# Performance work log

Measured on AMD Instinct MI355X. Metric: run time of the kernel, lower is better.

The kernel has to match this reference:

```python
import jax, jax.numpy as jnp
import numpy as np
import math

B, T, D, H, L, V = 2, 1024, 768, 12, 4, 50257
HD = D // H
ROPE_PCT = 0.5
MAX_WL = 10000.0
EPS = 1e-5


def setup_inputs() -> dict:
    key = jax.random.key(0)
    ks = jax.random.split(key, 8)
    s = 0.02
    return {
        "idx": jax.random.randint(ks[0], (B, T), 0, V, dtype=jnp.int32),
        "wte": jax.random.normal(ks[1], (V, D), jnp.float32) * s,
        "ln1_g": jnp.ones((L, D), jnp.float32),
        "ln1_b": jnp.zeros((L, D), jnp.float32),
        "Wqkv": jax.random.normal(ks[2], (L, D, 3 * D), jnp.float32) * s,
        "bqkv": jnp.zeros((L, 3 * D), jnp.float32),
        "Wo": jax.random.normal(ks[3], (L, D, D), jnp.float32) * s,
        "bo": jnp.zeros((L, D), jnp.float32),
        "ln2_g": jnp.ones((L, D), jnp.float32),
        "ln2_b": jnp.zeros((L, D), jnp.float32),
        "Wfc": jax.random.normal(ks[4], (L, D, 4 * D), jnp.float32) * s,
        "bfc": jnp.zeros((L, 4 * D), jnp.float32),
        "Wp": jax.random.normal(ks[5], (L, 4 * D, D), jnp.float32) * s,
        "bp": jnp.zeros((L, D), jnp.float32),
        "lnf_g": jnp.ones((D,), jnp.float32),
        "lnf_b": jnp.zeros((D,), jnp.float32),
        "Wlm": jax.random.normal(ks[6], (D, V), jnp.float32) * s,
    }


def _ln(x, g, b):
    m = x.mean(-1, keepdims=True)
    v = x.var(-1, keepdims=True)
    return (x - m) / jnp.sqrt(v + EPS) * g + b


def _gelu(x):
    return 0.5 * x * (1.0 + jnp.tanh(math.sqrt(2.0 / math.pi) * (x + 0.044715 * x ** 3)))


def _p_rope(x, positions):
    # x: [B, H, T, HD]; partial RoPE: rotate first ROPE_PCT of angle pairs, leave rest.
    rope_angles = int(ROPE_PCT * HD // 2)
    nope_angles = HD // 2 - rope_angles
    fraction = 2.0 * jnp.arange(0, rope_angles) / HD
    timescale = jnp.power(MAX_WL, fraction)
    timescale = jnp.pad(timescale, (0, nope_angles), constant_values=jnp.inf)
    sinusoid = positions[:, None] / timescale[None, :]  # [T, HD//2]; pos/inf = 0 -> no rotation
    sin, cos = jnp.sin(sinusoid), jnp.cos(sinusoid)
    first, second = jnp.split(x, 2, axis=-1)
    out = jnp.concatenate([first * cos - second * sin, second * cos + first * sin], axis=-1)
    return out.astype(x.dtype)


def reference(idx, wte, ln1_g, ln1_b, Wqkv, bqkv, Wo, bo, ln2_g, ln2_b, Wfc, bfc, Wp, bp, lnf_g, lnf_b, Wlm):
    x = wte[idx]  # [B, T, D]
    positions = jnp.arange(T, dtype=x.dtype)
    causal = jnp.tril(jnp.ones((T, T), dtype=bool))
    scale = jnp.sqrt(jnp.float32(HD)).astype(x.dtype)
    for l in range(L):
        h1 = _ln(x, ln1_g[l], ln1_b[l])
        h2 = _ln(x, ln2_g[l], ln2_b[l])  # note: both LNs read the same x (as in source)
        # attention
        qkv = h1 @ Wqkv[l] + bqkv[l]
        q, k, v = jnp.split(qkv, 3, axis=-1)
        sh = lambda t: t.reshape(B, T, H, HD).transpose(0, 2, 1, 3)
        q, k, v = sh(q), sh(k), sh(v)
        q = _p_rope(q, positions)
        k = _p_rope(k, positions)
        att = jnp.einsum('bhqd,bhkd->bhqk', q, k) / scale
        att = jnp.where(causal, att, jnp.finfo(att.dtype).min)
        att = jax.nn.softmax(att, axis=-1)
        y = jnp.einsum('bhqk,bhkd->bhqd', att, v)
        y = y.transpose(0, 2, 1, 3).reshape(B, T, D)
        x = x + (y @ Wo[l] + bo[l])
        # MLP
        h = _gelu(h2 @ Wfc[l] + bfc[l])
        x = x + (h @ Wp[l] + bp[l])
    x = _ln(x, lnf_g, lnf_b)
    logits = x @ Wlm  # [B, T, V]
    return logits
```

## Files before the change

### kernel.cpp

```cpp
#include <hip/hip_runtime.h>

typedef unsigned short u16;
typedef unsigned int u32;
typedef __attribute__((ext_vector_type(8))) short bf16x8;
typedef __attribute__((ext_vector_type(4))) float f32x4;

#define SEQ 1024
#define DM 768
#define NH 12
#define HD2 64
#define NLAYER 4
#define NVOCAB 50257
#define BT 2048

__device__ __forceinline__ u16 f2bf(float f) {
  union { float f; u32 u; } v; v.f = f;
  u32 r = v.u + 0x7FFFu + ((v.u >> 16) & 1u);
  return (u16)(r >> 16);
}
__device__ __forceinline__ float bf2f(u16 u) {
  union { u32 u; float f; } v; v.u = ((u32)u) << 16;
  return v.f;
}

__device__ __forceinline__ void glds16(const u16* g, u16* l) {
  __builtin_amdgcn_global_load_lds(
      (const __attribute__((address_space(1))) u32*)(const void*)g,
      (__attribute__((address_space(3))) u32*)(void*)l, 16, 0, 0);
}

__device__ __forceinline__ void cvt_tile(const float* __restrict__ in,
                                         u16* __restrict__ out, int R, int C,
                                         int cx, int ry, u16 (*t)[68]) {
  int c0 = cx * 64, r0 = ry * 64;
  int tx = threadIdx.x & 15, ty = threadIdx.x >> 4;
  int c = c0 + tx * 4;
#pragma unroll
  for (int i = 0; i < 4; ++i) {
    int r = r0 + ty + i * 16;
    float4 v = make_float4(0.f, 0.f, 0.f, 0.f);
    if (c + 3 < C) {
      v = *(const float4*)&in[(size_t)r * C + c];
    } else {
      if (c + 0 < C) v.x = in[(size_t)r * C + c];
      if (c + 1 < C) v.y = in[(size_t)r * C + c + 1];
      if (c + 2 < C) v.z = in[(size_t)r * C + c + 2];
      if (c + 3 < C) v.w = in[(size_t)r * C + c + 3];
    }
    t[ty + i * 16][tx * 4 + 0] = f2bf(v.x);
    t[ty + i * 16][tx * 4 + 1] = f2bf(v.y);
    t[ty + i * 16][tx * 4 + 2] = f2bf(v.z);
    t[ty + i * 16][tx * 4 + 3] = f2bf(v.w);
  }
  __syncthreads();
  int wl = threadIdx.x & 31, grp = threadIdx.x >> 5;
#pragma unroll
  for (int it = 0; it < 8; ++it) {
    int cc = it * 8 + grp;
    int gcol = c0 + cc;
    if (gcol < C) {
      u32 wv = (u32)t[2 * wl][cc] | ((u32)t[2 * wl + 1][cc] << 16);
      *(u32*)&out[(size_t)gcol * R + r0 + 2 * wl] = wv;
    }
  }
}

__global__ void k_prep(const int* __restrict__ idx, const float* __restrict__ wte,
                       float* __restrict__ xf, float* __restrict__ ctab,
                       float* __restrict__ stab, const float* __restrict__ Wqkv,
                       const float* __restrict__ Wo, const float* __restrict__ Wfc,
                       const float* __restrict__ Wp, const float* __restrict__ Wlm,
                       u16* __restrict__ wqkvT, u16* __restrict__ woT,
                       u16* __restrict__ wfcT, u16* __restrict__ wpT,
                       u16* __restrict__ wlmT) {
  __shared__ u16 t[64][68];
  int bid = blockIdx.x;
  if (bid < BT) {
    int tok = idx[bid];
    const float* s = wte + (size_t)tok * DM;
    float* d = xf + (size_t)bid * DM;
    for (int c = threadIdx.x; c < DM; c += 256) d[c] = s[c];
    return;
  }
  bid -= BT;
  if (bid < 64) {
    int gid = bid * 256 + threadIdx.x;
    int tt = gid >> 4, j = gid & 15;
    float inv = powf(10000.f, -(float)j * (1.f / 32.f));
    float ang = (float)tt * inv;
    ctab[gid] = cosf(ang);
    stab[gid] = sinf(ang);
    return;
  }
  bid -= 64;
  if (bid < NLAYER * 1728) {
    int layer = bid / 1728, r = bid % 1728;
    if (r < 432) {
      cvt_tile(Wqkv + (size_t)layer * DM * 3 * DM,
               wqkvT + (size_t)layer * 3 * DM * DM, DM, 3 * DM, r % 36, r / 36, t);
      return;
    }
    r -= 432;
    if (r < 144) {
      cvt_tile(Wo + (size_t)layer * DM * DM, woT + (size_t)layer * DM * DM,
               DM, DM, r % 12, r / 12, t);
      return;
    }
    r -= 144;
    if (r < 576) {
      cvt_tile(Wfc + (size_t)layer * DM * 4 * DM,
               wfcT + (size_t)layer * 4 * DM * DM, DM, 4 * DM, r % 48, r / 48, t);
      return;
    }
    r -= 576;
    cvt_tile(Wp + (size_t)layer * 4 * DM * DM, wpT + (size_t)layer * 4 * DM * DM,
             4 * DM, DM, r % 12, r / 12, t);
    return;
  }
  bid -= NLAYER * 1728;
  cvt_tile(Wlm, wlmT, DM, NVOCAB, bid % 786, bid / 786, t);
}

__global__ void k_ln(const float* __restrict__ x, const float* __restrict__ g1,
                     const float* __restrict__ b1, const float* __restrict__ g2,
                     const float* __restrict__ b2, u16* __restrict__ o1,
                     u16* __restrict__ o2) {
  int w = threadIdx.x >> 6, l = threadIdx.x & 63;
  int r = blockIdx.x * 4 + w;
  const float* xr = x + (size_t)r * DM;
  float2 v[6];
  float s = 0.f;
#pragma unroll
  for (int i = 0; i < 6; ++i) {
    v[i] = *(const float2*)&xr[2 * l + i * 128];
    s += v[i].x + v[i].y;
  }
#pragma unroll
  for (int o = 1; o < 64; o <<= 1) s += __shfl_xor(s, o);
  float mean = s * (1.f / DM);
  float vs = 0.f;
#pragma unroll
  for (int i = 0; i < 6; ++i) {
    float dx = v[i].x - mean, dy = v[i].y - mean;
    vs += dx * dx + dy * dy;
  }
#pragma unroll
  for (int o = 1; o < 64; o <<= 1) vs += __shfl_xor(vs, o);
  float rstd = rsqrtf(vs * (1.f / DM) + 1e-5f);
  u16* p1 = o1 + (size_t)r * DM;
#pragma unroll
  for (int i = 0; i < 6; ++i) {
    int c = 2 * l + i * 128;
    float2 gg = *(const float2*)&g1[c];
    float2 bb = *(const float2*)&b1[c];
    u32 wv = (u32)f2bf((v[i].x - mean) * rstd * gg.x + bb.x) |
             ((u32)f2bf((v[i].y - mean) * rstd * gg.y + bb.y) << 16);
    *(u32*)&p1[c] = wv;
  }
  if (o2) {
    u16* p2 = o2 + (size_t)r * DM;
#pragma unroll
    for (int i = 0; i < 6; ++i) {
      int c = 2 * l + i * 128;
      float2 gg = *(const float2*)&g2[c];
      float2 bb = *(const float2*)&b2[c];
      u32 wv = (u32)f2bf((v[i].x - mean) * rstd * gg.x + bb.x) |
               ((u32)f2bf((v[i].y - mean) * rstd * gg.y + bb.y) << 16);
      *(u32*)&p2[c] = wv;
    }
  }
}

__global__ void k_attn(const u16* __restrict__ qr, const u16* __restrict__ kr,
                       const u16* __restrict__ vT, u16* __restrict__ yb) {
  int ti = (int)gridDim.x - 1 - (int)blockIdx.x;
  int bh = blockIdx.y;
  __shared__ u16 Ps[64 * 72];
  __shared__ u16 Ks[2][4096];
  __shared__ u16 Vs[2][4096];
  int tid = threadIdx.x;
  int rr = tid >> 2, cc = tid & 3;
  int w = tid >> 6, l = tid & 63;
  int rl = l & 15, g = l >> 4;
  {
    const u16* gq = qr + ((size_t)bh * SEQ + ti * 64 + rr) * HD2;
    *(uint4*)&Ps[rr * 72 + cc * 8]      = *(const uint4*)(gq + cc * 8);
    *(uint4*)&Ps[rr * 72 + cc * 8 + 32] = *(const uint4*)(gq + cc * 8 + 32);
  }
  int srow = w * 8 + (l >> 3);
  int gs = (l & 7) ^ (l >> 3);
  const u16* gkb = kr + (size_t)bh * SEQ * HD2;
  const u16* gvb = vT + (size_t)bh * HD2 * SEQ;
  glds16(gkb + (size_t)srow * 64 + gs * 8,        &Ks[0][w * 512]);
  glds16(gkb + (size_t)(32 + srow) * 64 + gs * 8, &Ks[0][2048 + w * 512]);
  glds16(gvb + (size_t)srow * SEQ + gs * 8,       &Vs[0][w * 512]);
  glds16(gvb + (size_t)(32 + srow) * SEQ + gs * 8,&Vs[0][2048 + w * 512]);
  __syncthreads();
  bf16x8 aq0 = *(const bf16x8*)&Ps[(w * 16 + rl) * 72 + g * 8];
  bf16x8 aq1 = *(const bf16x8*)&Ps[(w * 16 + rl) * 72 + 32 + g * 8];
  float m[4], lsum[4];
  f32x4 oacc[4] = {};
#pragma unroll
  for (int r2 = 0; r2 < 4; ++r2) { m[r2] = -3.0e38f; lsum[r2] = 0.f; }
  int qloc = w * 16 + g * 4;
  int sw = rl & 7;
  int cur = 0;
  for (int kt = 0; kt <= ti; ++kt) {
    if (kt < ti) {
      int nx = cur ^ 1;
      glds16(gkb + (size_t)((kt + 1) * 64 + srow) * 64 + gs * 8,      &Ks[nx][w * 512]);
      glds16(gkb + (size_t)((kt + 1) * 64 + 32 + srow) * 64 + gs * 8, &Ks[nx][2048 + w * 512]);
      glds16(gvb + (size_t)srow * SEQ + (kt + 1) * 64 + gs * 8,       &Vs[nx][w * 512]);
      glds16(gvb + (size_t)(32 + srow) * SEQ + (kt + 1) * 64 + gs * 8,&Vs[nx][2048 + w * 512]);
    }
    f32x4 s[4] = {};
    __builtin_amdgcn_s_setprio(1);
#pragma unroll
    for (int nt = 0; nt < 4; ++nt) {
      int r = (nt * 16 + rl) * 64;
      bf16x8 b0 = *(const bf16x8*)&Ks[cur][r + ((0 + g) ^ sw) * 8];
      bf16x8 b1 = *(const bf16x8*)&Ks[cur][r + ((4 + g) ^ sw) * 8];
      s[nt] = __builtin_amdgcn_mfma_f32_16x16x32_bf16(aq0, b0, s[nt], 0, 0, 0);
      s[nt] = __builtin_amdgcn_mfma_f32_16x16x32_bf16(aq1, b1, s[nt], 0, 0, 0);
    }
    __builtin_amdgcn_s_setprio(0);
    if (kt == ti) {
#pragma unroll
      for (int nt = 0; nt < 4; ++nt) {
        int col = nt * 16 + rl;
#pragma unroll
        for (int r2 = 0; r2 < 4; ++r2)
          if (col > qloc + r2) s[nt][r2] = -3.0e38f;
      }
    }
    float lmax[4];
#pragma unroll
    for (int r2 = 0; r2 < 4; ++r2)
      lmax[r2] = fmaxf(fmaxf(s[0][r2], s[1][r2]), fmaxf(s[2][r2], s[3][r2]));
    bool need = (lmax[0] > m[0] + 8.f) || (lmax[1] > m[1] + 8.f) ||
                (lmax[2] > m[2] + 8.f) || (lmax[3] > m[3] + 8.f);
    if (__any(need)) {
#pragma unroll
      for (int r2 = 0; r2 < 4; ++r2) {
        float pm = lmax[r2];
#pragma unroll
        for (int o = 1; o < 16; o <<= 1) pm = fmaxf(pm, __shfl_xor(pm, o));
        if (pm > m[r2] + 8.f) {
          float corr = __expf(m[r2] - pm);
          m[r2] = pm;
          lsum[r2] *= corr;
          oacc[0][r2] *= corr; oacc[1][r2] *= corr;
          oacc[2][r2] *= corr; oacc[3][r2] *= corr;
        }
      }
    }
#pragma unroll
    for (int r2 = 0; r2 < 4; ++r2) {
      float p0 = __expf(s[0][r2] - m[r2]);
      float p1 = __expf(s[1][r2] - m[r2]);
      float p2 = __expf(s[2][r2] - m[r2]);
      float p3 = __expf(s[3][r2] - m[r2]);
      float ps = p0 + p1 + p2 + p3;
#pragma unroll
      for (int o = 1; o < 16; o <<= 1) ps += __shfl_xor(ps, o);
      lsum[r2] += ps;
      int prow = (qloc + r2) * 72;
      Ps[prow + rl]      = f2bf(p0);
      Ps[prow + 16 + rl] = f2bf(p1);
      Ps[prow + 32 + rl] = f2bf(p2);
      Ps[prow + 48 + rl] = f2bf(p3);
    }
    bf16x8 pa0 = *(const bf16x8*)&Ps[(w * 16 + rl) * 72 + g * 8];
    bf16x8 pa1 = *(const bf16x8*)&Ps[(w * 16 + rl) * 72 + 32 + g * 8];
    __builtin_amdgcn_s_setprio(1);
#pragma unroll
    for (int nt = 0; nt < 4; ++nt) {
      int r = (nt * 16 + rl) * 64;
      bf16x8 b0 = *(const bf16x8*)&Vs[cur][r + ((0 + g) ^ sw) * 8];
      bf16x8 b1 = *(const bf16x8*)&Vs[cur][r + ((4 + g) ^ sw) * 8];
      oacc[nt] = __builtin_amdgcn_mfma_f32_16x16x32_bf16(pa0, b0, oacc[nt], 0, 0, 0);
      oacc[nt] = __builtin_amdgcn_mfma_f32_16x16x32_bf16(pa1, b1, oacc[nt], 0, 0, 0);
    }
    __builtin_amdgcn_s_setprio(0);
    __syncthreads();
    cur ^= 1;
  }
  int b = bh / NH, h = bh % NH;
  float invl[4];
#pragma unroll
  for (int r2 = 0; r2 < 4; ++r2) invl[r2] = 1.f / lsum[r2];
#pragma unroll
  for (int nt = 0; nt < 4; ++nt) {
    int d = nt * 16 + rl;
#pragma unroll
    for (int r2 = 0; r2 < 4; ++r2) {
      int trow = ti * 64 + qloc + r2;
      yb[((size_t)(b * SEQ + trow)) * DM + h * HD2 + d] = f2bf(oacc[nt][r2] * invl[r2]);
    }
  }
}

template <int MODE>
__global__ void k_g128(const u16* __restrict__ A, const u16* __restrict__ Bt,
                       float* __restrict__ outf, int M, int N, int K, int MT) {
  __shared__ u16 SM[16384];
  float* cw = (float*)SM;
  int nwg = gridDim.x;
  int id = blockIdx.x;
  if ((nwg & 7) == 0) id = (id & 7) * (nwg >> 3) + (id >> 3);
  int mt = id % MT, nt = id / MT;
  int m0 = mt * 128, n0 = nt * 128;
  int tid = threadIdx.x;
  int w = tid >> 6, l = tid & 63;
  int srow = w * 16 + (l >> 2);
  int gs = (l & 3) ^ ((l >> 3) & 3);
  const u16* gA0 = A + (size_t)(m0 + srow) * K + gs * 8;
  const u16* gA1 = A + (size_t)(m0 + 64 + srow) * K + gs * 8;
  int rb0 = n0 + srow;      if (rb0 > N - 1) rb0 = N - 1;
  int rb1 = n0 + 64 + srow; if (rb1 > N - 1) rb1 = N - 1;
  const u16* gB0 = Bt + (size_t)rb0 * K + gs * 8;
  const u16* gB1 = Bt + (size_t)rb1 * K + gs * 8;
  int wm = (w >> 1) * 64, wn = (w & 1) * 64;
  int rl = l & 15, g = l >> 4;
  int sla = g ^ ((rl >> 1) & 3);
  f32x4 acc[4][4] = {};
  int nK = K >> 5;
  int cur = 0;
  {
    u16* dA = SM + w * 512;
    glds16(gA0, dA); glds16(gA1, dA + 2048);
    u16* dB = SM + 4096 + w * 512;
    glds16(gB0, dB); glds16(gB1, dB + 2048);
  }
  __syncthreads();
  for (int kt = 0; kt < nK; ++kt) {
    if (kt + 1 < nK) {
      u16* dA = SM + (cur ^ 1) * 8192 + w * 512;
      glds16(gA0 + (kt + 1) * 32, dA); glds16(gA1 + (kt + 1) * 32, dA + 2048);
      u16* dB = dA + 4096;
      glds16(gB0 + (kt + 1) * 32, dB); glds16(gB1 + (kt + 1) * 32, dB + 2048);
    }
    const u16* As = SM + cur * 8192;
    const u16* Bs = As + 4096;
    bf16x8 af[4], bfr[4];
    __builtin_amdgcn_s_setprio(1);
#pragma unroll
    for (int i = 0; i < 4; ++i)
      af[i] = *(const bf16x8*)&As[(wm + i * 16 + rl) * 32 + sla * 8];
#pragma unroll
    for (int j = 0; j < 4; ++j)
      bfr[j] = *(const bf16x8*)&Bs[(wn + j * 16 + rl) * 32 + sla * 8];
#pragma unroll
    for (int i = 0; i < 4; ++i)
#pragma unroll
      for (int j = 0; j < 4; ++j)
        acc[i][j] = __builtin_amdgcn_mfma_f32_16x16x32_bf16(af[i], bfr[j],
                                                            acc[i][j], 0, 0, 0);
    __builtin_amdgcn_s_setprio(0);
    __syncthreads();
    cur ^= 1;
  }
#pragma unroll
  for (int ch = 0; ch < 4; ++ch) {
    if ((w >> 1) == (ch >> 1)) {
      int ib = (ch & 1) * 2;
#pragma unroll
      for (int ii = 0; ii < 2; ++ii) {
#pragma unroll
        for (int j = 0; j < 4; ++j) {
          int col = wn + j * 16 + rl;
#pragma unroll
          for (int r2 = 0; r2 < 4; ++r2) {
            int rowc = ii * 16 + g * 4 + r2;
            cw[rowc * 132 + col] = acc[ib + ii][j][r2];
          }
        }
      }
    }
    __syncthreads();
    for (int t = tid; t < 4096; t += 256) {
      int rowc = t >> 7, col = t & 127;
      int gc = n0 + col;
      if (gc < N)
        __builtin_nontemporal_store(cw[rowc * 132 + col],
                                    &outf[(size_t)(m0 + ch * 32 + rowc) * N + gc]);
    }
    __syncthreads();
  }
}

template <int MODE>
__global__ void k_gw(const u16* __restrict__ A, const u16* __restrict__ Bt,
                     const float* __restrict__ bias, u16* __restrict__ outb,
                     int M, int N, int K, int MT,
                     const float* __restrict__ ctab,
                     const float* __restrict__ stab, u16* __restrict__ qrp,
                     u16* __restrict__ krp, u16* __restrict__ vTp) {
  __shared__ u16 SM2[24576];
  float* cw = (float*)SM2;
  int nwg = gridDim.x;
  int id = blockIdx.x;
  if ((nwg & 7) == 0) id = (id & 7) * (nwg >> 3) + (id >> 3);
  int mt = id % MT, nt = id / MT;
  int m0 = mt * 64, n0 = nt * 128;
  int tid = threadIdx.x;
  int w = tid >> 6, l = tid & 63;
  int row0 = tid >> 3, slot0 = tid & 7;
  int gs0 = slot0 ^ (row0 & 7);
  const u16* gA0 = A + (size_t)(m0 + row0) * K + gs0 * 8;
  const u16* gA1 = gA0 + (size_t)32 * K;
  const u16* gB0 = Bt + (size_t)(n0 + row0) * K + gs0 * 8;
  const u16* gB1 = gB0 + (size_t)32 * K;
  const u16* gB2 = gB0 + (size_t)64 * K;
  const u16* gB3 = gB0 + (size_t)96 * K;
  int wm = (w >> 1) * 32, wn = (w & 1) * 64;
  int rl = l & 15, g = l >> 4;
  int sl0 = g ^ (rl & 7), sl1 = (4 + g) ^ (rl & 7);
  f32x4 acc[2][4] = {};
  int nK = K >> 6;
  int cur = 0;
  {
    u16* dA = SM2;
    glds16(gA0, dA + w * 512); glds16(gA1, dA + 2048 + w * 512);
    u16* dB = SM2 + 8192;
    glds16(gB0, dB + w * 512);        glds16(gB1, dB + 2048 + w * 512);
    glds16(gB2, dB + 4096 + w * 512); glds16(gB3, dB + 6144 + w * 512);
  }
  __syncthreads();
  for (int kt = 0; kt < nK; ++kt) {
    if (kt + 1 < nK) {
      int ka = (kt + 1) * 64;
      u16* dA = SM2 + (cur ^ 1) * 4096;
      glds16(gA0 + ka, dA + w * 512); glds16(gA1 + ka, dA + 2048 + w * 512);
      u16* dB = SM2 + 8192 + (cur ^ 1) * 8192;
      glds16(gB0 + ka, dB + w * 512);        glds16(gB1 + ka, dB + 2048 + w * 512);
      glds16(gB2 + ka, dB + 4096 + w * 512); glds16(gB3 + ka, dB + 6144 + w * 512);
    }
    const u16* Ac = SM2 + cur * 4096;
    const u16* Bc = SM2 + 8192 + cur * 8192;
    bf16x8 a0[2], a1[2], b0[4], b1[4];
    __builtin_amdgcn_s_setprio(1);
#pragma unroll
    for (int i = 0; i < 2; ++i) {
      int r = (wm + i * 16 + rl) * 64;
      a0[i] = *(const bf16x8*)&Ac[r + sl0 * 8];
      a1[i] = *(const bf16x8*)&Ac[r + sl1 * 8];
    }
#pragma unroll
    for (int j = 0; j < 4; ++j) {
      int r = (wn + j * 16 + rl) * 64;
      b0[j] = *(const bf16x8*)&Bc[r + sl0 * 8];
      b1[j] = *(const bf16x8*)&Bc[r + sl1 * 8];
    }
#pragma unroll
    for (int i = 0; i < 2; ++i)
#pragma unroll
      for (int j = 0; j < 4; ++j) {
        acc[i][j] = __builtin_amdgcn_mfma_f32_16x16x32_bf16(a0[i], b0[j],
                                                            acc[i][j], 0, 0, 0);
        acc[i][j] = __builtin_amdgcn_mfma_f32_16x16x32_bf16(a1[i], b1[j],
                                                            acc[i][j], 0, 0, 0);
      }
    __builtin_amdgcn_s_setprio(0);
    __syncthreads();
    cur ^= 1;
  }
#pragma unroll
  for (int i = 0; i < 2; ++i) {
#pragma unroll
    for (int j = 0; j < 4; ++j) {
      int col = wn + j * 16 + rl;
      float bv = bias[n0 + col];
#pragma unroll
      for (int r2 = 0; r2 < 4; ++r2) {
        float v = acc[i][j][r2] + bv;
        if (MODE == 1) {
          float u = 0.7978845608028654f * (v + 0.044715f * v * v * v);
          v = 0.5f * v * (1.f + tanhf(u));
        }
        cw[(wm + i * 16 + g * 4 + r2) * 133 + col] = v;
      }
    }
  }
  __syncthreads();
  if (MODE == 1) {
    for (int t = tid; t < 4096; t += 256) {
      int rowc = t >> 6, cp = t & 63;
      u32 wv = (u32)f2bf(cw[rowc * 133 + 2 * cp]) |
               ((u32)f2bf(cw[rowc * 133 + 2 * cp + 1]) << 16);
      *(u32*)&outb[(size_t)(m0 + rowc) * N + n0 + 2 * cp] = wv;
    }
  } else {
    int reg = n0 / DM;
    int h0 = (n0 % DM) / 64;
    int bb = m0 >> 10;
    int t0 = m0 & (SEQ - 1);
    size_t bhb = (size_t)bb * NH + h0;
    if (reg < 2) {
      u16* dst = (reg == 0) ? qrp : krp;
      float qs = (reg == 0) ? 0.125f : 1.f;
      for (int t = tid; t < 4096; t += 256) {
        int rowc = t >> 6, cp = t & 63;
        int c = 2 * cp;
        int hh = c >> 6, d = c & 63;
        int tt = t0 + rowc;
        float x0 = cw[rowc * 133 + c];
        float x1 = cw[rowc * 133 + c + 1];
        float o0, o1;
        if (d < 32) {
          float y0 = cw[rowc * 133 + c + 32];
          float y1 = cw[rowc * 133 + c + 33];
          float c0 = 1.f, s0 = 0.f, c1 = 1.f, s1 = 0.f;
          if (d < 16) {
            c0 = ctab[tt * 16 + d];     s0 = stab[tt * 16 + d];
            c1 = ctab[tt * 16 + d + 1]; s1 = stab[tt * 16 + d + 1];
          }
          o0 = x0 * c0 - y0 * s0;
          o1 = x1 * c1 - y1 * s1;
        } else {
          int j = d - 32;
          float y0 = cw[rowc * 133 + c - 32];
          float y1 = cw[rowc * 133 + c - 31];
          float c0 = 1.f, s0 = 0.f, c1 = 1.f, s1 = 0.f;
          if (j < 16) {
            c0 = ctab[tt * 16 + j];     s0 = stab[tt * 16 + j];
            c1 = ctab[tt * 16 + j + 1]; s1 = stab[tt * 16 + j + 1];
          }
          o0 = x0 * c0 + y0 * s0;
          o1 = x1 * c1 + y1 * s1;
        }
        u32 wv = (u32)f2bf(o0 * qs) | ((u32)f2bf(o1 * qs) << 16);
        *(u32*)&dst[((bhb + hh) * SEQ + tt) * HD2 + d] = wv;
      }
    } else {
      for (int t = tid; t < 4096; t += 256) {
        int dcol = t >> 5, p = t & 31;
        int hh = dcol >> 6, d = dcol & 63;
        int tt = t0 + 2 * p;
        u32 wv = (u32)f2bf(cw[(2 * p) * 133 + dcol]) |
                 ((u32)f2bf(cw[(2 * p + 1) * 133 + dcol]) << 16);
        *(u32*)&vTp[((bhb + hh) * HD2 + d) * SEQ + tt] = wv;
      }
    }
  }
}

__global__ void k_wofc(const u16* __restrict__ yb, const u16* __restrict__ woT,
                       const float* __restrict__ bo, float* __restrict__ xf,
                       const u16* __restrict__ h2b, const u16* __restrict__ wfcT,
                       const float* __restrict__ bfc, u16* __restrict__ hgel) {
  __shared__ u16 SM2[24576];
  int nwg = gridDim.x;
  int id = blockIdx.x;
  id = (id & 7) * (nwg >> 3) + (id >> 3);
  int tid = threadIdx.x;
  int w = tid >> 6, l = tid & 63;
  int rl = l & 15, g = l >> 4;
  int row0 = tid >> 3, slot0 = tid & 7;
  int gs0 = slot0 ^ (row0 & 7);
  int sl0 = g ^ (rl & 7), sl1 = (4 + g) ^ (rl & 7);
  if (id < 768) {
    float* cw = (float*)SM2;
    int mt = id % 32, nt = id / 32;
    int m0 = mt * 64, n0 = nt * 128;
    const int K = DM, N = 4 * DM;
    const u16* gA0 = h2b + (size_t)(m0 + row0) * K + gs0 * 8;
    const u16* gA1 = gA0 + (size_t)32 * K;
    const u16* gB0 = wfcT + (size_t)(n0 + row0) * K + gs0 * 8;
    const u16* gB1 = gB0 + (size_t)32 * K;
    const u16* gB2 = gB0 + (size_t)64 * K;
    const u16* gB3 = gB0 + (size_t)96 * K;
    int wm = (w >> 1) * 32, wn = (w & 1) * 64;
    f32x4 acc[2][4] = {};
    int nK = K >> 6;
    int cur = 0;
    {
      u16* dA = SM2;
      glds16(gA0, dA + w * 512); glds16(gA1, dA + 2048 + w * 512);
      u16* dB = SM2 + 8192;
      glds16(gB0, dB + w * 512);        glds16(gB1, dB + 2048 + w * 512);
      glds16(gB2, dB + 4096 + w * 512); glds16(gB3, dB + 6144 + w * 512);
    }
    __syncthreads();
    for (int kt = 0; kt < nK; ++kt) {
      if (kt + 1 < nK) {
        int ka = (kt + 1) * 64;
        u16* dA = SM2 + (cur ^ 1) * 4096;
        glds16(gA0 + ka, dA + w * 512); glds16(gA1 + ka, dA + 2048 + w * 512);
        u16* dB = SM2 + 8192 + (cur ^ 1) * 8192;
        glds16(gB0 + ka, dB + w * 512);        glds16(gB1 + ka, dB + 2048 + w * 512);
        glds16(gB2 + ka, dB + 4096 + w * 512); glds16(gB3 + ka, dB + 6144 + w * 512);
      }
      const u16* Ac = SM2 + cur * 4096;
      const u16* Bc = SM2 + 8192 + cur * 8192;
      bf16x8 a0[2], a1[2], b0[4], b1[4];
      __builtin_amdgcn_s_setprio(1);
#pragma unroll
      for (int i = 0; i < 2; ++i) {
        int r = (wm + i * 16 + rl) * 64;
        a0[i] = *(const bf16x8*)&Ac[r + sl0 * 8];
        a1[i] = *(const bf16x8*)&Ac[r + sl1 * 8];
      }
#pragma unroll
      for (int j = 0; j < 4; ++j) {
        int r = (wn + j * 16 + rl) * 64;
        b0[j] = *(const bf16x8*)&Bc[r + sl0 * 8];
        b1[j] = *(const bf16x8*)&Bc[r + sl1 * 8];
      }
#pragma unroll
      for (int i = 0; i < 2; ++i)
#pragma unroll
        for (int j = 0; j < 4; ++j) {
          acc[i][j] = __builtin_amdgcn_mfma_f32_16x16x32_bf16(a0[i], b0[j],
                                                              acc[i][j], 0, 0, 0);
          acc[i][j] = __builtin_amdgcn_mfma_f32_16x16x32_bf16(a1[i], b1[j],
                                                              acc[i][j], 0, 0, 0);
        }
      __builtin_amdgcn_s_setprio(0);
      __syncthreads();
      cur ^= 1;
    }
#pragma unroll
    for (int i = 0; i < 2; ++i) {
#pragma unroll
      for (int j = 0; j < 4; ++j) {
        int col = wn + j * 16 + rl;
        float bv = bfc[n0 + col];
#pragma unroll
        for (int r2 = 0; r2 < 4; ++r2) {
          float v = acc[i][j][r2] + bv;
          float u = 0.7978845608028654f * (v + 0.044715f * v * v * v);
          v = 0.5f * v * (1.f + tanhf(u));
          cw[(wm + i * 16 + g * 4 + r2) * 133 + col] = v;
        }
      }
    }
    __syncthreads();
    for (int t = tid; t < 4096; t += 256) {
      int rowc = t >> 6, cp = t & 63;
      u32 wv = (u32)f2bf(cw[rowc * 133 + 2 * cp]) |
               ((u32)f2bf(cw[rowc * 133 + 2 * cp + 1]) << 16);
      *(u32*)&hgel[(size_t)(m0 + rowc) * N + n0 + 2 * cp] = wv;
    }
    return;
  }
  {
    int id2 = id - 768;
    int sk = id2 / 384, t = id2 % 384;
    int mt = t % 32, nt = t / 32;
    int m0 = mt * 64, n0 = nt * 64;
    const int K = DM, N = DM;
    int Kc = K / 2, k0 = sk * Kc;
    u16* As = SM2;
    u16* Bs = SM2 + 8192;
    const u16* gA0 = yb + (size_t)(m0 + row0) * K + k0 + gs0 * 8;
    const u16* gA1 = gA0 + (size_t)32 * K;
    const u16* gB0 = woT + (size_t)(n0 + row0) * K + k0 + gs0 * 8;
    const u16* gB1 = gB0 + (size_t)32 * K;
    int wm = (w >> 1) * 32, wn = (w & 1) * 32;
    f32x4 acc[2][2] = {};
    int nK = Kc >> 6;
    int cur = 0;
    {
      glds16(gA0, As + w * 512); glds16(gA1, As + 2048 + w * 512);
      glds16(gB0, Bs + w * 512); glds16(gB1, Bs + 2048 + w * 512);
    }
    __syncthreads();
    for (int kt = 0; kt < nK; ++kt) {
      if (kt + 1 < nK) {
        int nx = (cur ^ 1) * 4096;
        glds16(gA0 + (kt + 1) * 64, As + nx + w * 512);
        glds16(gA1 + (kt + 1) * 64, As + nx + 2048 + w * 512);
        glds16(gB0 + (kt + 1) * 64, Bs + nx + w * 512);
        glds16(gB1 + (kt + 1) * 64, Bs + nx + 2048 + w * 512);
      }
      const u16* Ac = As + cur * 4096;
      const u16* Bc = Bs + cur * 4096;
      bf16x8 a0[2], a1[2], b0[2], b1[2];
      __builtin_amdgcn_s_setprio(1);
#pragma unroll
      for (int i = 0; i < 2; ++i) {
        int r = (wm + i * 16 + rl) * 64;
        a0[i] = *(const bf16x8*)&Ac[r + sl0 * 8];
        a1[i] = *(const bf16x8*)&Ac[r + sl1 * 8];
      }
#pragma unroll
      for (int j = 0; j < 2; ++j) {
        int r = (wn + j * 16 + rl) * 64;
        b0[j] = *(const bf16x8*)&Bc[r + sl0 * 8];
        b1[j] = *(const bf16x8*)&Bc[r + sl1 * 8];
      }
#pragma unroll
      for (int i = 0; i < 2; ++i)
#pragma unroll
        for (int j = 0; j < 2; ++j) {
          acc[i][j] = __builtin_amdgcn_mfma_f32_16x16x32_bf16(a0[i], b0[j],
                                                              acc[i][j], 0, 0, 0);
          acc[i][j] = __builtin_amdgcn_mfma_f32_16x16x32_bf16(a1[i], b1[j],
                                                              acc[i][j], 0, 0, 0);
        }
      __builtin_amdgcn_s_setprio(0);
      __syncthreads();
      cur ^= 1;
    }
#pragma unroll
    for (int i = 0; i < 2; ++i) {
#pragma unroll
      for (int j = 0; j < 2; ++j) {
        int col = n0 + wn + j * 16 + rl;
        float bv = bo[col];
#pragma unroll
        for (int r2 = 0; r2 < 4; ++r2) {
          int row = m0 + wm + i * 16 + g * 4 + r2;
          float v = acc[i][j][r2];
          if (sk == 0) v += bv;
          atomicAdd(&xf[(size_t)row * N + col], v);
        }
      }
    }
  }
}

__global__ void k_g64r(const u16* __restrict__ A, const u16* __restrict__ Bt,
                       const float* __restrict__ bias,
                       float* __restrict__ outf, int M, int N, int K, int MT) {
  __shared__ u16 As[8192];
  __shared__ u16 Bs[8192];
  int nwg = gridDim.x;
  int id = blockIdx.x;
  if ((nwg & 7) == 0) id = (id & 7) * (nwg >> 3) + (id >> 3);
  int mt = id % MT, nt = id / MT;
  int sk = blockIdx.y, nsk = gridDim.y;
  int Kc = K / nsk, k0 = sk * Kc;
  int m0 = mt * 64, n0 = nt * 64;
  int tid = threadIdx.x;
  int w = tid >> 6, l = tid & 63;
  int row0 = tid >> 3, slot0 = tid & 7;
  int gs0 = slot0 ^ (row0 & 7);
  const u16* gA0 = A + (size_t)(m0 + row0) * K + k0 + gs0 * 8;
  const u16* gA1 = gA0 + (size_t)32 * K;
  const u16* gB0 = Bt + (size_t)(n0 + row0) * K + k0 + gs0 * 8;
  const u16* gB1 = gB0 + (size_t)32 * K;
  int wm = (w >> 1) * 32, wn = (w & 1) * 32;
  int rl = l & 15, g = l >> 4;
  int sl0 = g ^ (rl & 7), sl1 = (4 + g) ^ (rl & 7);
  f32x4 acc[2][2] = {};
  int nK = Kc >> 6;
  int cur = 0;
  {
    glds16(gA0, As + w * 512); glds16(gA1, As + 2048 + w * 512);
    glds16(gB0, Bs + w * 512); glds16(gB1, Bs + 2048 + w * 512);
  }
  __syncthreads();
  for (int kt = 0; kt < nK; ++kt) {
    if (kt + 1 < nK) {
      int nx = (cur ^ 1) * 4096;
      glds16(gA0 + (kt + 1) * 64, As + nx + w * 512);
      glds16(gA1 + (kt + 1) * 64, As + nx + 2048 + w * 512);
      glds16(gB0 + (kt + 1) * 64, Bs + nx + w * 512);
      glds16(gB1 + (kt + 1) * 64, Bs + nx + 2048 + w * 512);
    }
    const u16* Ac = As + cur * 4096;
    const u16* Bc = Bs + cur * 4096;
    bf16x8 a0[2], a1[2], b0[2], b1[2];
    __builtin_amdgcn_s_setprio(1);
#pragma unroll
    for (int i = 0; i < 2; ++i) {
      int r = (wm + i * 16 + rl) * 64;
      a0[i] = *(const bf16x8*)&Ac[r + sl0 * 8];
      a1[i] = *(const bf16x8*)&Ac[r + sl1 * 8];
    }
#pragma unroll
    for (int j = 0; j < 2; ++j) {
      int r = (wn + j * 16 + rl) * 64;
      b0[j] = *(const bf16x8*)&Bc[r + sl0 * 8];
      b1[j] = *(const bf16x8*)&Bc[r + sl1 * 8];
    }
#pragma unroll
    for (int i = 0; i < 2; ++i)
#pragma unroll
      for (int j = 0; j < 2; ++j) {
        acc[i][j] = __builtin_amdgcn_mfma_f32_16x16x32_bf16(a0[i], b0[j],
                                                            acc[i][j], 0, 0, 0);
        acc[i][j] = __builtin_amdgcn_mfma_f32_16x16x32_bf16(a1[i], b1[j],
                                                            acc[i][j], 0, 0, 0);
      }
    __builtin_amdgcn_s_setprio(0);
    __syncthreads();
    cur ^= 1;
  }
#pragma unroll
  for (int i = 0; i < 2; ++i) {
#pragma unroll
    for (int j = 0; j < 2; ++j) {
      int col = n0 + wn + j * 16 + rl;
      float bv = bias ? bias[col] : 0.f;
#pragma unroll
      for (int r2 = 0; r2 < 4; ++r2) {
        int row = m0 + wm + i * 16 + g * 4 + r2;
        float v = acc[i][j][r2];
        if (sk == 0) v += bv;
        atomicAdd(&outf[(size_t)row * N + col], v);
      }
    }
  }
}

__global__ void k_gemm_f32b(const u16* __restrict__ A, const float* __restrict__ B,
                            float* __restrict__ outf, int M, int N, int K) {
  __shared__ u16 As[128 * 40];
  __shared__ u16 Bs[4 * 128 * 12];
  int tid = threadIdx.x;
  int wid = tid >> 6, lane = tid & 63;
  int rl = lane & 15, g = lane >> 4;
  int m0 = blockIdx.x * 128, n0 = blockIdx.y * 128;
  int wm = (wid >> 1) * 64, wn = (wid & 1) * 64;
  int ar = tid >> 2, ac = tid & 3;
  int bn = tid & 127, bq = tid >> 7;
  f32x4 acc[4][4] = {};
  int nK = K / 32;
  for (int kt = 0; kt < nK; ++kt) {
    __syncthreads();
    {
      const u16* ga = A + (size_t)(m0 + ar) * K + kt * 32 + ac * 8;
      *(uint4*)&As[ar * 40 + ac * 8] = *(const uint4*)ga;
      *(uint4*)&As[(ar + 64) * 40 + ac * 8] = *(const uint4*)(ga + (size_t)64 * K);
    }
    int col = n0 + bn;
#pragma unroll
    for (int r = 0; r < 4; ++r) {
      int kq = bq + 2 * r;
      int kk = kt * 32 + kq * 4;
      float f0 = 0.f, f1 = 0.f, f2v = 0.f, f3 = 0.f;
      if (col < N) {
        const float* gb = B + (size_t)kk * N + col;
        f0 = gb[0]; f1 = gb[(size_t)N]; f2v = gb[(size_t)2 * N]; f3 = gb[(size_t)3 * N];
      }
      uint2 wv;
      wv.x = (u32)f2bf(f0) | ((u32)f2bf(f1) << 16);
      wv.y = (u32)f2bf(f2v) | ((u32)f2bf(f3) << 16);
      *(uint2*)&Bs[(kq >> 1) * 1536 + bn * 12 + (kq & 1) * 4] = wv;
    }
    __syncthreads();
    bf16x8 af[4], bfr[4];
#pragma unroll
    for (int mt = 0; mt < 4; ++mt)
      af[mt] = *(const bf16x8*)&As[(wm + mt * 16 + rl) * 40 + g * 8];
#pragma unroll
    for (int nt = 0; nt < 4; ++nt) {
      const u16* p = &Bs[g * 1536 + (wn + nt * 16 + rl) * 12];
      union { bf16x8 v; uint2 u2[2]; } tmp;
      tmp.u2[0] = *(const uint2*)p;
      tmp.u2[1] = *(const uint2*)(p + 4);
      bfr[nt] = tmp.v;
    }
#pragma unroll
    for (int mt = 0; mt < 4; ++mt)
#pragma unroll
      for (int nt = 0; nt < 4; ++nt)
        acc[mt][nt] = __builtin_amdgcn_mfma_f32_16x16x32_bf16(af[mt], bfr[nt],
                                                              acc[mt][nt], 0, 0, 0);
  }
#pragma unroll
  for (int mt = 0; mt < 4; ++mt)
#pragma unroll
    for (int nt = 0; nt < 4; ++nt) {
      int col = n0 + wn + nt * 16 + rl;
      if (col >= N) continue;
#pragma unroll
      for (int r2 = 0; r2 < 4; ++r2) {
        int row = m0 + wm + mt * 16 + g * 4 + r2;
        outf[(size_t)row * N + col] = acc[mt][nt][r2];
      }
    }
}

extern "C" void kernel_launch(void* const* d_in, const int* in_sizes, int n_in,
                              void* d_out, int out_size, void* d_ws, size_t ws_size,
                              hipStream_t stream) {
  (void)in_sizes; (void)n_in; (void)out_size;
  const int*   idx  = (const int*)  d_in[0];
  const float* wte  = (const float*)d_in[1];
  const float* ln1g = (const float*)d_in[2];
  const float* ln1b = (const float*)d_in[3];
  const float* Wqkv = (const float*)d_in[4];
  const float* bqkv = (const float*)d_in[5];
  const float* Wo   = (const float*)d_in[6];
  const float* bo   = (const float*)d_in[7];
  const float* ln2g = (const float*)d_in[8];
  const float* ln2b = (const float*)d_in[9];
  const float* Wfc  = (const float*)d_in[10];
  const float* bfc  = (const float*)d_in[11];
  const float* Wp   = (const float*)d_in[12];
  const float* bp   = (const float*)d_in[13];
  const float* lnfg = (const float*)d_in[14];
  const float* lnfb = (const float*)d_in[15];
  const float* Wlm  = (const float*)d_in[16];
  float* out = (float*)d_out;

  char* sb = (char*)d_out;
  size_t off = 0;
  auto alloc = [&](size_t bytes) {
    char* p = sb + off;
    off += (bytes + 255) & ~(size_t)255;
    return (void*)p;
  };
  float* xf  = (float*)alloc((size_t)BT * DM * 4);
  u16* h1b   = (u16*)alloc((size_t)BT * DM * 2);
  u16* h2b   = (u16*)alloc((size_t)BT * DM * 2);
  u16* qr    = (u16*)alloc((size_t)BT * DM * 2);
  u16* kr    = (u16*)alloc((size_t)BT * DM * 2);
  u16* vT    = (u16*)alloc((size_t)BT * DM * 2);
  u16* yb    = (u16*)alloc((size_t)BT * DM * 2);
  u16* hgel  = (u16*)alloc((size_t)BT * 4 * DM * 2);
  float* ctab = (float*)alloc((size_t)SEQ * 16 * 4);
  float* stab = (float*)alloc((size_t)SEQ * 16 * 4);
  u16* wqkvT = (u16*)alloc((size_t)NLAYER * 3 * DM * DM * 2);
  u16* woT   = (u16*)alloc((size_t)NLAYER * DM * DM * 2);
  u16* wfcT  = (u16*)alloc((size_t)NLAYER * 4 * DM * DM * 2);
  u16* wpT   = (u16*)alloc((size_t)NLAYER * 4 * DM * DM * 2);

  size_t wlmT_bytes = (size_t)NVOCAB * DM * 2;
  size_t xlnf_bytes = (size_t)BT * DM * 2;
  bool fast_lm = ws_size >= wlmT_bytes + xlnf_bytes + 512;
  u16* wlmT = (u16*)d_ws;
  u16* xlnf = fast_lm ? (u16*)((char*)d_ws + ((wlmT_bytes + 255) & ~(size_t)255))
                      : (u16*)d_ws;

  int prep_blocks = BT + 64 + NLAYER * 1728 + (fast_lm ? 9432 : 0);
  k_prep<<<prep_blocks, 256, 0, stream>>>(idx, wte, xf, ctab, stab,
                                          Wqkv, Wo, Wfc, Wp, Wlm,
                                          wqkvT, woT, wfcT, wpT, wlmT);

  for (int l = 0; l < NLAYER; ++l) {
    k_ln<<<BT / 4, 256, 0, stream>>>(xf, ln1g + l * DM, ln1b + l * DM,
                                     ln2g + l * DM, ln2b + l * DM, h1b, h2b);
    k_gw<4><<<(BT / 64) * (3 * DM / 128), 256, 0, stream>>>(
        h1b, wqkvT + (size_t)l * 3 * DM * DM, bqkv + (size_t)l * 3 * DM,
        nullptr, BT, 3 * DM, DM, BT / 64, ctab, stab, qr, kr, vT);
    k_attn<<<dim3(SEQ / 64, 2 * NH), 256, 0, stream>>>(qr, kr, vT, yb);
    k_wofc<<<1536, 256, 0, stream>>>(
        yb, woT + (size_t)l * DM * DM, bo + (size_t)l * DM, xf,
        h2b, wfcT + (size_t)l * 4 * DM * DM, bfc + (size_t)l * 4 * DM, hgel);
    k_g64r<<<dim3((BT / 64) * (DM / 64), 4), 256, 0, stream>>>(
        hgel, wpT + (size_t)l * 4 * DM * DM, bp + (size_t)l * DM, xf, BT, DM, 4 * DM,
        BT / 64);
  }
  k_ln<<<BT / 4, 256, 0, stream>>>(xf, lnfg, lnfb, nullptr, nullptr, xlnf, nullptr);
  if (fast_lm) {
    int nt = (NVOCAB + 127) / 128;
    k_g128<3><<<(BT / 128) * nt, 256, 0, stream>>>(
        xlnf, wlmT, out, BT, NVOCAB, DM, BT / 128);
  } else {
    k_gemm_f32b<<<dim3(BT / 128, (NVOCAB + 127) / 128), 256, 0, stream>>>(
        xlnf, Wlm, out, BT, NVOCAB, DM);
  }
}
```

Baseline: 876.8 us.

## Pair complementary causal query tiles per attention block to balance work

Each attention workgroup now handles two query tiles (p and 15-p), so every block does the same number of KV steps. The K/V tiles loaded for the longer tile are shared with the shorter one, which halves KV traffic for the shared range. The grid shrinks from 16x24 to 8x24 blocks (192), which may leave many compute units idle on a large GPU. Each block also holds twice the accumulator registers and more shared memory.

```diff
diff --git a/kernel.cpp b/kernel.cpp
--- a/kernel.cpp
+++ b/kernel.cpp
@@ -173,9 +173,11 @@
 
 __global__ void k_attn(const u16* __restrict__ qr, const u16* __restrict__ kr,
                        const u16* __restrict__ vT, u16* __restrict__ yb) {
-  int ti = (int)gridDim.x - 1 - (int)blockIdx.x;
+  int p = blockIdx.x;
   int bh = blockIdx.y;
-  __shared__ u16 Ps[64 * 72];
+  int tA = 15 - p, tB = p;
+  __shared__ u16 PsA[64 * 72];
+  __shared__ u16 PsB[64 * 72];
   __shared__ u16 Ks[2][4096];
   __shared__ u16 Vs[2][4096];
   int tid = threadIdx.x;
@@ -183,9 +185,12 @@
   int w = tid >> 6, l = tid & 63;
   int rl = l & 15, g = l >> 4;
   {
-    const u16* gq = qr + ((size_t)bh * SEQ + ti * 64 + rr) * HD2;
-    *(uint4*)&Ps[rr * 72 + cc * 8]      = *(const uint4*)(gq + cc * 8);
-    *(uint4*)&Ps[rr * 72 + cc * 8 + 32] = *(const uint4*)(gq + cc * 8 + 32);
+    const u16* gqA = qr + ((size_t)bh * SEQ + tA * 64 + rr) * HD2;
+    const u16* gqB = qr + ((size_t)bh * SEQ + tB * 64 + rr) * HD2;
+    *(uint4*)&PsA[rr * 72 + cc * 8]      = *(const uint4*)(gqA + cc * 8);
+    *(uint4*)&PsA[rr * 72 + cc * 8 + 32] = *(const uint4*)(gqA + cc * 8 + 32);
+    *(uint4*)&PsB[rr * 72 + cc * 8]      = *(const uint4*)(gqB + cc * 8);
+    *(uint4*)&PsB[rr * 72 + cc * 8 + 32] = *(const uint4*)(gqB + cc * 8 + 32);
   }
   int srow = w * 8 + (l >> 3);
   int gs = (l & 7) ^ (l >> 3);
@@ -196,106 +201,183 @@
   glds16(gvb + (size_t)srow * SEQ + gs * 8,       &Vs[0][w * 512]);
   glds16(gvb + (size_t)(32 + srow) * SEQ + gs * 8,&Vs[0][2048 + w * 512]);
   __syncthreads();
-  bf16x8 aq0 = *(const bf16x8*)&Ps[(w * 16 + rl) * 72 + g * 8];
-  bf16x8 aq1 = *(const bf16x8*)&Ps[(w * 16 + rl) * 72 + 32 + g * 8];
-  float m[4], lsum[4];
-  f32x4 oacc[4] = {};
-#pragma unroll
-  for (int r2 = 0; r2 < 4; ++r2) { m[r2] = -3.0e38f; lsum[r2] = 0.f; }
+  bf16x8 aqA0 = *(const bf16x8*)&PsA[(w * 16 + rl) * 72 + g * 8];
+  bf16x8 aqA1 = *(const bf16x8*)&PsA[(w * 16 + rl) * 72 + 32 + g * 8];
+  bf16x8 aqB0 = *(const bf16x8*)&PsB[(w * 16 + rl) * 72 + g * 8];
+  bf16x8 aqB1 = *(const bf16x8*)&PsB[(w * 16 + rl) * 72 + 32 + g * 8];
+  float mA[4], lsA[4], mB[4], lsB[4];
+  f32x4 oA[4] = {}, oB[4] = {};
+#pragma unroll
+  for (int r2 = 0; r2 < 4; ++r2) {
+    mA[r2] = -3.0e38f; lsA[r2] = 0.f;
+    mB[r2] = -3.0e38f; lsB[r2] = 0.f;
+  }
   int qloc = w * 16 + g * 4;
   int sw = rl & 7;
   int cur = 0;
-  for (int kt = 0; kt <= ti; ++kt) {
-    if (kt < ti) {
+  for (int kt = 0; kt <= tA; ++kt) {
+    if (kt < tA) {
       int nx = cur ^ 1;
       glds16(gkb + (size_t)((kt + 1) * 64 + srow) * 64 + gs * 8,      &Ks[nx][w * 512]);
       glds16(gkb + (size_t)((kt + 1) * 64 + 32 + srow) * 64 + gs * 8, &Ks[nx][2048 + w * 512]);
       glds16(gvb + (size_t)srow * SEQ + (kt + 1) * 64 + gs * 8,       &Vs[nx][w * 512]);
       glds16(gvb + (size_t)(32 + srow) * SEQ + (kt + 1) * 64 + gs * 8,&Vs[nx][2048 + w * 512]);
     }
-    f32x4 s[4] = {};
-    __builtin_amdgcn_s_setprio(1);
-#pragma unroll
-    for (int nt = 0; nt < 4; ++nt) {
-      int r = (nt * 16 + rl) * 64;
-      bf16x8 b0 = *(const bf16x8*)&Ks[cur][r + ((0 + g) ^ sw) * 8];
-      bf16x8 b1 = *(const bf16x8*)&Ks[cur][r + ((4 + g) ^ sw) * 8];
-      s[nt] = __builtin_amdgcn_mfma_f32_16x16x32_bf16(aq0, b0, s[nt], 0, 0, 0);
-      s[nt] = __builtin_amdgcn_mfma_f32_16x16x32_bf16(aq1, b1, s[nt], 0, 0, 0);
-    }
-    __builtin_amdgcn_s_setprio(0);
-    if (kt == ti) {
+    {
+      f32x4 s[4] = {};
+      __builtin_amdgcn_s_setprio(1);
 #pragma unroll
       for (int nt = 0; nt < 4; ++nt) {
-        int col = nt * 16 + rl;
-#pragma unroll
-        for (int r2 = 0; r2 < 4; ++r2)
-          if (col > qloc + r2) s[nt][r2] = -3.0e38f;
-      }
-    }
-    float lmax[4];
-#pragma unroll
-    for (int r2 = 0; r2 < 4; ++r2)
-      lmax[r2] = fmaxf(fmaxf(s[0][r2], s[1][r2]), fmaxf(s[2][r2], s[3][r2]));
-    bool need = (lmax[0] > m[0] + 8.f) || (lmax[1] > m[1] + 8.f) ||
-                (lmax[2] > m[2] + 8.f) || (lmax[3] > m[3] + 8.f);
-    if (__any(need)) {
+        int r = (nt * 16 + rl) * 64;
+        bf16x8 b0 = *(const bf16x8*)&Ks[cur][r + ((0 + g) ^ sw) * 8];
+        bf16x8 b1 = *(const bf16x8*)&Ks[cur][r + ((4 + g) ^ sw) * 8];
+        s[nt] = __builtin_amdgcn_mfma_f32_16x16x32_bf16(aqA0, b0, s[nt], 0, 0, 0);
+        s[nt] = __builtin_amdgcn_mfma_f32_16x16x32_bf16(aqA1, b1, s[nt], 0, 0, 0);
+      }
+      __builtin_amdgcn_s_setprio(0);
+      if (kt == tA) {
+#pragma unroll
+        for (int nt = 0; nt < 4; ++nt) {
+          int col = nt * 16 + rl;
+#pragma unroll
+          for (int r2 = 0; r2 < 4; ++r2)
+            if (col > qloc + r2) s[nt][r2] = -3.0e38f;
+        }
+      }
+      float lmax[4];
+#pragma unroll
+      for (int r2 = 0; r2 < 4; ++r2)
+        lmax[r2] = fmaxf(fmaxf(s[0][r2], s[1][r2]), fmaxf(s[2][r2], s[3][r2]));
+      bool need = (lmax[0] > mA[0] + 8.f) || (lmax[1] > mA[1] + 8.f) ||
+                  (lmax[2] > mA[2] + 8.f) || (lmax[3] > mA[3] + 8.f);
+      if (__any(need)) {
+#pragma unroll
+        for (int r2 = 0; r2 < 4; ++r2) {
+          float pm = lmax[r2];
+#pragma unroll
+          for (int o = 1; o < 16; o <<= 1) pm = fmaxf(pm, __shfl_xor(pm, o));
+          if (pm > mA[r2] + 8.f) {
+            float corr = __expf(mA[r2] - pm);
+            mA[r2] = pm;
+            lsA[r2] *= corr;
+            oA[0][r2] *= corr; oA[1][r2] *= corr;
+            oA[2][r2] *= corr; oA[3][r2] *= corr;
+          }
+        }
+      }
 #pragma unroll
       for (int r2 = 0; r2 < 4; ++r2) {
-        float pm = lmax[r2];
-#pragma unroll
-        for (int o = 1; o < 16; o <<= 1) pm = fmaxf(pm, __shfl_xor(pm, o));
-        if (pm > m[r2] + 8.f) {
-          float corr = __expf(m[r2] - pm);
-          m[r2] = pm;
-          lsum[r2] *= corr;
-          oacc[0][r2] *= corr; oacc[1][r2] *= corr;
-          oacc[2][r2] *= corr; oacc[3][r2] *= corr;
+        float p0 = __expf(s[0][r2] - mA[r2]);
+        float p1 = __expf(s[1][r2] - mA[r2]);
+        float p2 = __expf(s[2][r2] - mA[r2]);
+        float p3 = __expf(s[3][r2] - mA[r2]);
+        float ps = p0 + p1 + p2 + p3;
+#pragma unroll
+        for (int o = 1; o < 16; o <<= 1) ps += __shfl_xor(ps, o);
+        lsA[r2] += ps;
+        int prow = (qloc + r2) * 72;
+        PsA[prow + rl]      = f2bf(p0);
+        PsA[prow + 16 + rl] = f2bf(p1);
+        PsA[prow + 32 + rl] = f2bf(p2);
+        PsA[prow + 48 + rl] = f2bf(p3);
+      }
+      bf16x8 pa0 = *(const bf16x8*)&PsA[(w * 16 + rl) * 72 + g * 8];
+      bf16x8 pa1 = *(const bf16x8*)&PsA[(w * 16 + rl) * 72 + 32 + g * 8];
+      __builtin_amdgcn_s_setprio(1);
+#pragma unroll
+      for (int nt = 0; nt < 4; ++nt) {
+        int r = (nt * 16 + rl) * 64;
+        bf16x8 b0 = *(const bf16x8*)&Vs[cur][r + ((0 + g) ^ sw) * 8];
+        bf16x8 b1 = *(const bf16x8*)&Vs[cur][r + ((4 + g) ^ sw) * 8];
+        oA[nt] = __builtin_amdgcn_mfma_f32_16x16x32_bf16(pa0, b0, oA[nt], 0, 0, 0);
+        oA[nt] = __builtin_amdgcn_mfma_f32_16x16x32_bf16(pa1, b1, oA[nt], 0, 0, 0);
+      }
+      __builtin_amdgcn_s_setprio(0);
+    }
+    if (kt <= tB) {
+      f32x4 s[4] = {};
+      __builtin_amdgcn_s_setprio(1);
+#pragma unroll
+      for (int nt = 0; nt < 4; ++nt) {
+        int r = (nt * 16 + rl) * 64;
+        bf16x8 b0 = *(const bf16x8*)&Ks[cur][r + ((0 + g) ^ sw) * 8];
+        bf16x8 b1 = *(const bf16x8*)&Ks[cur][r + ((4 + g) ^ sw) * 8];
+        s[nt] = __builtin_amdgcn_mfma_f32_16x16x32_bf16(aqB0, b0, s[nt], 0, 0, 0);
+        s[nt] = __builtin_amdgcn_mfma_f32_16x16x32_bf16(aqB1, b1, s[nt], 0, 0, 0);
+      }
+      __builtin_amdgcn_s_setprio(0);
+      if (kt == tB) {
+#pragma unroll
+        for (int nt = 0; nt < 4; ++nt) {
+          int col = nt * 16 + rl;
+#pragma unroll
+          for (int r2 = 0; r2 < 4; ++r2)
+            if (col > qloc + r2) s[nt][r2] = -3.0e38f;
         }
       }
-    }
-#pragma unroll
-    for (int r2 = 0; r2 < 4; ++r2) {
-      float p0 = __expf(s[0][r2] - m[r2]);
-      float p1 = __expf(s[1][r2] - m[r2]);
-      float p2 = __expf(s[2][r2] - m[r2]);
-      float p3 = __expf(s[3][r2] - m[r2]);
-      float ps = p0 + p1 + p2 + p3;
-#pragma unroll
-      for (int o = 1; o < 16; o <<= 1) ps += __shfl_xor(ps, o);
-      lsum[r2] += ps;
-      int prow = (qloc + r2) * 72;
-      Ps[prow + rl]      = f2bf(p0);
-      Ps[prow + 16 + rl] = f2bf(p1);
-      Ps[prow + 32 + rl] = f2bf(p2);
-      Ps[prow + 48 + rl] = f2bf(p3);
-    }
-    bf16x8 pa0 = *(const bf16x8*)&Ps[(w * 16 + rl) * 72 + g * 8];
-    bf16x8 pa1 = *(const bf16x8*)&Ps[(w * 16 + rl) * 72 + 32 + g * 8];
-    __builtin_amdgcn_s_setprio(1);
-#pragma unroll
-    for (int nt = 0; nt < 4; ++nt) {
-      int r = (nt * 16 + rl) * 64;
-      bf16x8 b0 = *(const bf16x8*)&Vs[cur][r + ((0 + g) ^ sw) * 8];
-      bf16x8 b1 = *(const bf16x8*)&Vs[cur][r + ((4 + g) ^ sw) * 8];
-      oacc[nt] = __builtin_amdgcn_mfma_f32_16x16x32_bf16(pa0, b0, oacc[nt], 0, 0, 0);
-      oacc[nt] = __builtin_amdgcn_mfma_f32_16x16x32_bf16(pa1, b1, oacc[nt], 0, 0, 0);
-    }
-    __builtin_amdgcn_s_setprio(0);
+      float lmax[4];
+#pragma unroll
+      for (int r2 = 0; r2 < 4; ++r2)
+        lmax[r2] = fmaxf(fmaxf(s[0][r2], s[1][r2]), fmaxf(s[2][r2], s[3][r2]));
+      bool need = (lmax[0] > mB[0] + 8.f) || (lmax[1] > mB[1] + 8.f) ||
+                  (lmax[2] > mB[2] + 8.f) || (lmax[3] > mB[3] + 8.f);
+      if (__any(need)) {
+#pragma unroll
+        for (int r2 = 0; r2 < 4; ++r2) {
+          float pm = lmax[r2];
+#pragma unroll
+          for (int o = 1; o < 16; o <<= 1) pm = fmaxf(pm, __shfl_xor(pm, o));
+          if (pm > mB[r2] + 8.f) {
+            float corr = __expf(mB[r2] - pm);
+            mB[r2] = pm;
+            lsB[r2] *= corr;
+            oB[0][r2] *= corr; oB[1][r2] *= corr;
+            oB[2][r2] *= corr; oB[3][r2] *= corr;
+          }
+        }
+      }
+#pragma unroll
+      for (int r2 = 0; r2 < 4; ++r2) {
+        float p0 = __expf(s[0][r2] - mB[r2]);
+        float p1 = __expf(s[1][r2] - mB[r2]);
+        float p2 = __expf(s[2][r2] - mB[r2]);
+        float p3 = __expf(s[3][r2] - mB[r2]);
+        float ps = p0 + p1 + p2 + p3;
+#pragma unroll
+        for (int o = 1; o < 16; o <<= 1) ps += __shfl_xor(ps, o);
+        lsB[r2] += ps;
+        int prow = (qloc + r2) * 72;
+        PsB[prow + rl]      = f2bf(p0);
+        PsB[prow + 16 + rl] = f2bf(p1);
+        PsB[prow + 32 + rl] = f2bf(p2);
+        PsB[prow + 48 + rl] = f2bf(p3);
+      }
+      bf16x8 pb0 = *(const bf16x8*)&PsB[(w * 16 + rl) * 72 + g * 8];
+      bf16x8 pb1 = *(const bf16x8*)&PsB[(w * 16 + rl) * 72 + 32 + g * 8];
+      __builtin_amdgcn_s_setprio(1);
+#pragma unroll
+      for (int nt = 0; nt < 4; ++nt) {
+        int r = (nt * 16 + rl) * 64;
+        bf16x8 b0 = *(const bf16x8*)&Vs[cur][r + ((0 + g) ^ sw) * 8];
+        bf16x8 b1 = *(const bf16x8*)&Vs[cur][r + ((4 + g) ^ sw) * 8];
+        oB[nt] = __builtin_amdgcn_mfma_f32_16x16x32_bf16(pb0, b0, oB[nt], 0, 0, 0);
+        oB[nt] = __builtin_amdgcn_mfma_f32_16x16x32_bf16(pb1, b1, oB[nt], 0, 0, 0);
+      }
+      __builtin_amdgcn_s_setprio(0);
+    }
     __syncthreads();
     cur ^= 1;
   }
   int b = bh / NH, h = bh % NH;
-  float invl[4];
-#pragma unroll
-  for (int r2 = 0; r2 < 4; ++r2) invl[r2] = 1.f / lsum[r2];
 #pragma unroll
   for (int nt = 0; nt < 4; ++nt) {
     int d = nt * 16 + rl;
 #pragma unroll
     for (int r2 = 0; r2 < 4; ++r2) {
-      int trow = ti * 64 + qloc + r2;
-      yb[((size_t)(b * SEQ + trow)) * DM + h * HD2 + d] = f2bf(oacc[nt][r2] * invl[r2]);
+      int rowA = tA * 64 + qloc + r2;
+      int rowB = tB * 64 + qloc + r2;
+      yb[((size_t)(b * SEQ + rowA)) * DM + h * HD2 + d] = f2bf(oA[nt][r2] / lsA[r2]);
+      yb[((size_t)(b * SEQ + rowB)) * DM + h * HD2 + d] = f2bf(oB[nt][r2] / lsB[r2]);
     }
   }
 }
@@ -938,7 +1020,7 @@
     k_gw<4><<<(BT / 64) * (3 * DM / 128), 256, 0, stream>>>(
         h1b, wqkvT + (size_t)l * 3 * DM * DM, bqkv + (size_t)l * 3 * DM,
         nullptr, BT, 3 * DM, DM, BT / 64, ctab, stab, qr, kr, vT);
-    k_attn<<<dim3(SEQ / 64, 2 * NH), 256, 0, stream>>>(qr, kr, vT, yb);
+    k_attn<<<dim3(8, 2 * NH), 256, 0, stream>>>(qr, kr, vT, yb);
     k_wofc<<<1536, 256, 0, stream>>>(
         yb, woT + (size_t)l * DM * DM, bo + (size_t)l * DM, xf,
         h2b, wfcT + (size_t)l * 4 * DM * DM, bfc + (size_t)l * 4 * DM, hgel);
```

Measured after the change: 884.8 us. Within noise of the previous version (+0.9%).
